# Performance work log

Measured on AMD Instinct MI355X. Metric: run time of the kernel, lower is better.

## Reference

```python
import jax, jax.numpy as jnp
import numpy as np

LN_EPS = 1e-5


def setup_inputs() -> dict:
    key = jax.random.key(0)
    ks = jax.random.split(key, 8)
    B, L, d_model = 2, 2048, 1024
    d_inner, d_state, dt_rank, d_conv = 2048, 16, 64, 4
    f32 = jnp.float32
    A_init = jnp.broadcast_to(jnp.arange(1, d_state + 1, dtype=f32), (d_inner, d_state))
    return {
        "x": jax.random.normal(ks[0], (B, L, d_model), f32),
        "norm_g": jnp.ones((d_model,), f32),
        "norm_b": jnp.zeros((d_model,), f32),
        "in_w": jax.random.normal(ks[1], (2 * d_inner, d_model), f32) / np.sqrt(d_model),
        "conv_w": jax.random.normal(ks[2], (d_inner, 1, d_conv), f32) / np.sqrt(d_conv),
        "conv_b": jnp.zeros((d_inner,), f32),
        "xproj_w": jax.random.normal(ks[3], (dt_rank + 2 * d_state, d_inner), f32) / np.sqrt(d_inner),
        "dt_w": jax.random.normal(ks[4], (d_inner, dt_rank), f32) / np.sqrt(dt_rank),
        "dt_b": jax.random.uniform(ks[5], (d_inner,), f32, np.log(1e-4), np.log(0.1)),
        "A_log": jnp.log(A_init),
        "D": jnp.ones((d_inner,), f32),
        "out_w": jax.random.normal(ks[6], (d_model, d_inner), f32) / np.sqrt(d_inner),
    }


def reference(x, norm_g, norm_b, in_w, conv_w, conv_b, xproj_w, dt_w, dt_b, A_log, D, out_w):
    Bsz, L, d_model = x.shape
    d_inner, d_state = A_log.shape
    dt_rank = dt_w.shape[1]
    d_conv = conv_w.shape[-1]

    residual = x
    # LayerNorm
    mu = jnp.mean(x, axis=-1, keepdims=True)
    var = jnp.var(x, axis=-1, keepdims=True)
    xn = (x - mu) * jax.lax.rsqrt(var + LN_EPS) * norm_g + norm_b

    # in_proj and split into conv/SSM branch x_ and gate z
    xz = xn @ in_w.T                       # (B, L, 2*d_inner)
    x_, z = xz[..., :d_inner], xz[..., d_inner:]

    # causal depthwise conv1d (pad left d_conv-1, truncate to L)
    xp = jnp.pad(x_, ((0, 0), (d_conv - 1, 0), (0, 0)))
    w = conv_w[:, 0, :]                    # (d_inner, d_conv)
    xc = conv_b + sum(xp[:, k:k + L, :] * w[:, k] for k in range(d_conv))
    u = jax.nn.silu(xc)                    # (B, L, d_inner)

    # input-dependent SSM projections
    dbc = u @ xproj_w.T                    # (B, L, dt_rank + 2*d_state)
    delta_raw = dbc[..., :dt_rank]
    Bm = dbc[..., dt_rank:dt_rank + d_state]
    Cm = dbc[..., dt_rank + d_state:]
    delta = jax.nn.softplus(delta_raw @ dt_w.T + dt_b)  # (B, L, d_inner)
    A = -jnp.exp(A_log)                    # (d_inner, d_state), negative

    # selective scan over L (ZOH-discretized recurrence)
    def step(h, ins):
        d_t, B_t, C_t, u_t = ins           # (B,d_inner),(B,N),(B,N),(B,d_inner)
        dA = jnp.exp(d_t[..., None] * A)                 # (B, d_inner, N)
        dB = d_t[..., None] * B_t[:, None, :]            # (B, d_inner, N)
        h = dA * h + dB * u_t[..., None]
        y_t = jnp.einsum('bdn,bn->bd', h, C_t)
        return h, y_t

    h0 = jnp.zeros((Bsz, d_inner, d_state), x.dtype)
    xs = (jnp.swapaxes(delta, 0, 1), jnp.swapaxes(Bm, 0, 1),
          jnp.swapaxes(Cm, 0, 1), jnp.swapaxes(u, 0, 1))
    _, ys = jax.lax.scan(step, h0, xs)     # ys: (L, B, d_inner)
    y = jnp.swapaxes(ys, 0, 1) + u * D

    # gate, out projection, residual (dropout is identity in eval)
    y = y * jax.nn.silu(z)
    return y @ out_w.T + residual
```

## Files before the change

### kernel.cpp

```cpp
#include <hip/hip_runtime.h>
#include <stdint.h>

typedef unsigned short u16;
typedef unsigned int u32;
typedef __attribute__((ext_vector_type(8))) short bf16x8;
typedef __attribute__((ext_vector_type(4))) float f32x4;
typedef __attribute__((ext_vector_type(4))) unsigned short u16x4;

#define DEV static __device__ __forceinline__

DEV u16 f2b(float f) {
  u32 u = __builtin_bit_cast(u32, f);
  u32 r = (u + 0x7fffu + ((u >> 16) & 1u)) >> 16;
  return (u16)r;
}
DEV float b2f(u16 b) {
  u32 u = ((u32)b) << 16;
  return __builtin_bit_cast(float, u);
}

DEV float fexp2(float x) {
#if __has_builtin(__builtin_amdgcn_exp2f)
  return __builtin_amdgcn_exp2f(x);
#else
  float r;
  asm("v_exp_f32 %0, %1" : "=v"(r) : "v"(x));
  return r;
#endif
}
DEV float flog2(float x) {
#if __has_builtin(__builtin_amdgcn_logf)
  return __builtin_amdgcn_logf(x);
#else
  float r;
  asm("v_log_f32 %0, %1" : "=v"(r) : "v"(x));
  return r;
#endif
}
#define L2E 1.44269504f

DEV void gld16(const void* g, void* l) {
  __builtin_amdgcn_global_load_lds(
      (__attribute__((address_space(1))) void*)(void*)(g),
      (__attribute__((address_space(3))) void*)(l), 16, 0, 0);
}

__global__ void cvt_f32_bf16(const float* __restrict__ in, u16* __restrict__ out, int n) {
  int i = blockIdx.x * blockDim.x + threadIdx.x;
  int stride = gridDim.x * blockDim.x;
  for (; i < n; i += stride) out[i] = f2b(in[i]);
}

__global__ void cvt_pad_xproj(const float* __restrict__ in, u16* __restrict__ out) {
  int i = blockIdx.x * blockDim.x + threadIdx.x;
  int n = i >> 11;
  out[i] = (n < 96) ? f2b(in[i]) : (u16)0;
}

__global__ __launch_bounds__(256) void ln_fwd(const float* __restrict__ x,
                                              const float* __restrict__ g,
                                              const float* __restrict__ bb,
                                              u16* __restrict__ xn) {
  int row = blockIdx.x;
  int t = threadIdx.x;
  const float4 v = ((const float4*)(x + (size_t)row * 1024))[t];
  float s = v.x + v.y + v.z + v.w;
  float ss = fmaf(v.x, v.x, fmaf(v.y, v.y, fmaf(v.z, v.z, v.w * v.w)));
  for (int off = 32; off; off >>= 1) {
    s += __shfl_down(s, off);
    ss += __shfl_down(ss, off);
  }
  __shared__ float red[8];
  __shared__ float mv[2];
  int w = t >> 6;
  if ((t & 63) == 0) { red[w] = s; red[4 + w] = ss; }
  __syncthreads();
  if (t == 0) {
    float S = red[0] + red[1] + red[2] + red[3];
    float SS = red[4] + red[5] + red[6] + red[7];
    float mu = S * (1.f / 1024.f);
    float var = SS * (1.f / 1024.f) - mu * mu;
    mv[0] = mu;
    mv[1] = rsqrtf(var + 1e-5f);
  }
  __syncthreads();
  float mu = mv[0], rstd = mv[1];
  float4 gv = ((const float4*)g)[t];
  float4 bv = ((const float4*)bb)[t];
  u16x4 o;
  o.x = f2b((v.x - mu) * rstd * gv.x + bv.x);
  o.y = f2b((v.y - mu) * rstd * gv.y + bv.y);
  o.z = f2b((v.z - mu) * rstd * gv.z + bv.z);
  o.w = f2b((v.w - mu) * rstd * gv.w + bv.w);
  ((u16x4*)(xn + (size_t)row * 1024))[t] = o;
}

template <int EPI>
__global__ __launch_bounds__(256, 2) void gemm_bt(const u16* __restrict__ A,
                                                  const u16* __restrict__ Bw,
                                                  void* __restrict__ Cp,
                                                  const float* __restrict__ aux,
                                                  int M, int N, int K) {
  __shared__ u16 As[128 * 32];
  __shared__ u16 Bs[128 * 32];
  const int t = threadIdx.x;
  const int m0 = blockIdx.y * 128;
  const int n0 = blockIdx.x * 128;
  const int lane = t & 63;
  const int wv = t >> 6;
  const int wr = (wv >> 1) * 64;
  const int wc = (wv & 1) * 64;
  const int fr = lane & 15;
  const int fk = (lane >> 4) * 8;

  const int i0 = t, i1 = t + 256;
  const u16* ga0 = A + (size_t)(m0 + (i0 >> 2)) * K + (i0 & 3) * 8;
  const u16* ga1 = A + (size_t)(m0 + (i1 >> 2)) * K + (i1 & 3) * 8;
  const u16* gb0 = Bw + (size_t)(n0 + (i0 >> 2)) * K + (i0 & 3) * 8;
  const u16* gb1 = Bw + (size_t)(n0 + (i1 >> 2)) * K + (i1 & 3) * 8;
  u16* la0 = &As[i0 * 8];
  u16* la1 = &As[i1 * 8];
  u16* lb0 = &Bs[i0 * 8];
  u16* lb1 = &Bs[i1 * 8];

  f32x4 acc[4][4] = {};

  for (int k0 = 0; k0 < K; k0 += 32) {
    gld16(ga0 + k0, la0);
    gld16(ga1 + k0, la1);
    gld16(gb0 + k0, lb0);
    gld16(gb1 + k0, lb1);
    asm volatile("s_waitcnt vmcnt(0)" ::: "memory");
    __syncthreads();
    bf16x8 av[4], bv[4];
#pragma unroll
    for (int mi = 0; mi < 4; ++mi)
      av[mi] = *(const bf16x8*)&As[(wr + mi * 16 + fr) * 32 + fk];
#pragma unroll
    for (int ni = 0; ni < 4; ++ni)
      bv[ni] = *(const bf16x8*)&Bs[(wc + ni * 16 + fr) * 32 + fk];
#pragma unroll
    for (int mi = 0; mi < 4; ++mi)
#pragma unroll
      for (int ni = 0; ni < 4; ++ni)
        acc[mi][ni] = __builtin_amdgcn_mfma_f32_16x16x32_bf16(av[mi], bv[ni], acc[mi][ni], 0, 0, 0);
    __syncthreads();
  }

  const int orow = (lane >> 4) * 4;
  const int ocol = lane & 15;
#pragma unroll
  for (int mi = 0; mi < 4; ++mi)
#pragma unroll
    for (int ni = 0; ni < 4; ++ni)
#pragma unroll
      for (int r = 0; r < 4; ++r) {
        const int gr = m0 + wr + mi * 16 + orow + r;
        const int gc = n0 + wc + ni * 16 + ocol;
        const size_t off = (size_t)gr * N + gc;
        float v = acc[mi][ni][r];
        if (EPI == 0) {
          ((u16*)Cp)[off] = f2b(v);
        } else if (EPI == 1) {
          ((float*)Cp)[off] = v;
        } else if (EPI == 2) {
          float sx = v + aux[gc];
          float sp = (sx > 30.f) ? sx : 0.69314718f * flog2(1.f + fexp2(sx * L2E));
          ((float*)Cp)[off] = sp;
        } else {
          ((float*)Cp)[off] = v + aux[off];
        }
      }
}

__global__ __launch_bounds__(256, 2) void gemm_xproj_sk(const u16* __restrict__ A,
                                                        const u16* __restrict__ Bw,
                                                        float* __restrict__ part) {
  __shared__ u16 As[128 * 32];
  __shared__ u16 Bs[128 * 32];
  const int K = 2048, N = 128;
  const int t = threadIdx.x;
  const int m0 = blockIdx.y * 128;
  const int z = blockIdx.z;
  const int kbeg = z * 256, kend = kbeg + 256;
  const int lane = t & 63;
  const int wv = t >> 6;
  const int wr = (wv >> 1) * 64;
  const int wc = (wv & 1) * 64;
  const int fr = lane & 15;
  const int fk = (lane >> 4) * 8;

  const int i0 = t, i1 = t + 256;
  const u16* ga0 = A + (size_t)(m0 + (i0 >> 2)) * K + (i0 & 3) * 8;
  const u16* ga1 = A + (size_t)(m0 + (i1 >> 2)) * K + (i1 & 3) * 8;
  const u16* gb0 = Bw + (size_t)(i0 >> 2) * K + (i0 & 3) * 8;
  const u16* gb1 = Bw + (size_t)(i1 >> 2) * K + (i1 & 3) * 8;
  u16* la0 = &As[i0 * 8];
  u16* la1 = &As[i1 * 8];
  u16* lb0 = &Bs[i0 * 8];
  u16* lb1 = &Bs[i1 * 8];

  f32x4 acc[4][4] = {};

  for (int k0 = kbeg; k0 < kend; k0 += 32) {
    gld16(ga0 + k0, la0);
    gld16(ga1 + k0, la1);
    gld16(gb0 + k0, lb0);
    gld16(gb1 + k0, lb1);
    asm volatile("s_waitcnt vmcnt(0)" ::: "memory");
    __syncthreads();
    bf16x8 av[4], bv[4];
#pragma unroll
    for (int mi = 0; mi < 4; ++mi)
      av[mi] = *(const bf16x8*)&As[(wr + mi * 16 + fr) * 32 + fk];
#pragma unroll
    for (int ni = 0; ni < 4; ++ni)
      bv[ni] = *(const bf16x8*)&Bs[(wc + ni * 16 + fr) * 32 + fk];
#pragma unroll
    for (int mi = 0; mi < 4; ++mi)
#pragma unroll
      for (int ni = 0; ni < 4; ++ni)
        acc[mi][ni] = __builtin_amdgcn_mfma_f32_16x16x32_bf16(av[mi], bv[ni], acc[mi][ni], 0, 0, 0);
    __syncthreads();
  }

  const int orow = (lane >> 4) * 4;
  const int ocol = lane & 15;
  float* outp = part + (size_t)z * 4096 * 128;
#pragma unroll
  for (int mi = 0; mi < 4; ++mi)
#pragma unroll
    for (int ni = 0; ni < 4; ++ni)
#pragma unroll
      for (int r = 0; r < 4; ++r) {
        const int gr = m0 + wr + mi * 16 + orow + r;
        const int gc = wc + ni * 16 + ocol;
        outp[(size_t)gr * N + gc] = acc[mi][ni][r];
      }
}

__global__ __launch_bounds__(256) void reduce_xproj(const float* __restrict__ part,
                                                    float* __restrict__ dbc,
                                                    u16* __restrict__ dr) {
  int tid = blockIdx.x * 256 + threadIdx.x;
  int m = tid >> 7, col = tid & 127;
  float s = 0.f;
#pragma unroll
  for (int z = 0; z < 8; ++z) s += part[(size_t)z * 524288 + tid];
  dbc[tid] = s;
  if (col < 64) dr[m * 64 + col] = f2b(s);
}

__global__ __launch_bounds__(256) void conv_silu(const u16* __restrict__ xz,
                                                 const float* __restrict__ cw,
                                                 const float* __restrict__ cb,
                                                 u16* __restrict__ u) {
  int idx = blockIdx.x * 256 + threadIdx.x;
  int m = idx >> 9;
  int d = (idx & 511) << 2;
  int tt = m & 2047;
  float4 w0 = *(const float4*)&cw[(size_t)d * 4];
  float4 w1 = *(const float4*)&cw[(size_t)d * 4 + 4];
  float4 w2 = *(const float4*)&cw[(size_t)d * 4 + 8];
  float4 w3 = *(const float4*)&cw[(size_t)d * 4 + 12];
  float4 cbv = *(const float4*)&cb[d];
  float s0 = cbv.x, s1 = cbv.y, s2 = cbv.z, s3 = cbv.w;
#pragma unroll
  for (int k = 0; k < 4; ++k) {
    int ts = tt + k - 3;
    if (ts < 0) continue;
    u16x4 xv = *(const u16x4*)&xz[((size_t)(m + k - 3)) * 4096 + d];
    float wa = (k == 0) ? w0.x : (k == 1) ? w0.y : (k == 2) ? w0.z : w0.w;
    float wb = (k == 0) ? w1.x : (k == 1) ? w1.y : (k == 2) ? w1.z : w1.w;
    float wc = (k == 0) ? w2.x : (k == 1) ? w2.y : (k == 2) ? w2.z : w2.w;
    float wd = (k == 0) ? w3.x : (k == 1) ? w3.y : (k == 2) ? w3.z : w3.w;
    s0 = fmaf(b2f(xv.x), wa, s0);
    s1 = fmaf(b2f(xv.y), wb, s1);
    s2 = fmaf(b2f(xv.z), wc, s2);
    s3 = fmaf(b2f(xv.w), wd, s3);
  }
  s0 = s0 * __builtin_amdgcn_rcpf(1.f + fexp2(-s0 * L2E));
  s1 = s1 * __builtin_amdgcn_rcpf(1.f + fexp2(-s1 * L2E));
  s2 = s2 * __builtin_amdgcn_rcpf(1.f + fexp2(-s2 * L2E));
  s3 = s3 * __builtin_amdgcn_rcpf(1.f + fexp2(-s3 * L2E));
  u16x4 o;
  o.x = f2b(s0); o.y = f2b(s1); o.z = f2b(s2); o.w = f2b(s3);
  *(u16x4*)&u[(size_t)m * 2048 + d] = o;
}


__global__ __launch_bounds__(256, 4) void scan_pass1(const float* __restrict__ delta,
                                                     const u16* __restrict__ ub,
                                                     const float* __restrict__ dbc,
                                                     const float* __restrict__ A_log,
                                                     float* __restrict__ Sb,
                                                     float* __restrict__ Qb) {
  __shared__ float Bs[32 * 16];
  const int blk = blockIdx.x;
  const int b = blk >> 9;
  const int r = blk & 511;
  const int ch = r >> 3;
  const int g = r & 7;
  const int t = threadIdx.x;
  const int d = g * 256 + t;
  const size_t mbase = (size_t)b * 2048 + (size_t)ch * 32;
  {
    int row = t >> 3, pr = t & 7;
    const float2 v = *(const float2*)&dbc[(mbase + row) * 128 + 64 + pr * 2];
    *(float2*)&Bs[row * 16 + pr * 2] = v;
  }
  float AvL2E[16];
  {
    const float4* ap = (const float4*)(A_log + (size_t)d * 16);
#pragma unroll
    for (int q = 0; q < 4; ++q) {
      float4 a = ap[q];
      AvL2E[q * 4 + 0] = -__expf(a.x) * L2E;
      AvL2E[q * 4 + 1] = -__expf(a.y) * L2E;
      AvL2E[q * 4 + 2] = -__expf(a.z) * L2E;
      AvL2E[q * 4 + 3] = -__expf(a.w) * L2E;
    }
  }
  const float* dptr = delta + mbase * 2048 + d;
  const u16* uptr = ub + mbase * 2048 + d;
  float h[16];
#pragma unroll
  for (int n = 0; n < 16; ++n) h[n] = 0.f;
  float S = 0.f;
  __syncthreads();
#pragma unroll 4
  for (int i = 0; i < 32; ++i) {
    float dt = dptr[(size_t)i * 2048];
    float uu = b2f(uptr[(size_t)i * 2048]);
    S += dt;
    float c = dt * uu;
    f32x4 B0 = *(const f32x4*)&Bs[i * 16 + 0];
    f32x4 B1 = *(const f32x4*)&Bs[i * 16 + 4];
    f32x4 B2 = *(const f32x4*)&Bs[i * 16 + 8];
    f32x4 B3 = *(const f32x4*)&Bs[i * 16 + 12];
#pragma unroll
    for (int n = 0; n < 4; ++n) {
      h[n] = fmaf(fexp2(dt * AvL2E[n]), h[n], c * B0[n]);
      h[4 + n] = fmaf(fexp2(dt * AvL2E[4 + n]), h[4 + n], c * B1[n]);
      h[8 + n] = fmaf(fexp2(dt * AvL2E[8 + n]), h[8 + n], c * B2[n]);
      h[12 + n] = fmaf(fexp2(dt * AvL2E[12 + n]), h[12 + n], c * B3[n]);
    }
  }
  const size_t o = (((size_t)ch * 2 + b) * 2048 + d) * 16;
  float4* qp = (float4*)(Qb + o);
  qp[0] = make_float4(h[0], h[1], h[2], h[3]);
  qp[1] = make_float4(h[4], h[5], h[6], h[7]);
  qp[2] = make_float4(h[8], h[9], h[10], h[11]);
  qp[3] = make_float4(h[12], h[13], h[14], h[15]);
  Sb[((size_t)ch * 2 + b) * 2048 + d] = S;
}

__global__ __launch_bounds__(256) void scan_pass2(const float* __restrict__ A_log,
                                                  const float* __restrict__ Sb,
                                                  float* __restrict__ Qb) {
  const int tid = blockIdx.x * 256 + threadIdx.x;
  const int n = tid & 15;
  const int dd = (tid >> 4) & 2047;
  const int b = tid >> 15;
  const float AvL2E = -__expf(A_log[dd * 16 + n]) * L2E;
  float carry = 0.f;
  float Sc = Sb[(size_t)b * 2048 + dd];
  float Qc = Qb[((size_t)b * 2048 + dd) * 16 + n];
  for (int j = 0; j < 64; ++j) {
    float Sn = 0.f, Qn = 0.f;
    if (j + 1 < 64) {
      Sn = Sb[((size_t)(j + 1) * 2 + b) * 2048 + dd];
      Qn = Qb[(((size_t)(j + 1) * 2 + b) * 2048 + dd) * 16 + n];
    }
    float P = fexp2(AvL2E * Sc);
    Qb[(((size_t)j * 2 + b) * 2048 + dd) * 16 + n] = carry;
    carry = fmaf(P, carry, Qc);
    Sc = Sn;
    Qc = Qn;
  }
}

__global__ __launch_bounds__(256, 4) void scan_pass3(const float* __restrict__ delta,
                                                     const u16* __restrict__ ub,
                                                     const float* __restrict__ dbc,
                                                     const u16* __restrict__ xz,
                                                     const float* __restrict__ A_log,
                                                     const float* __restrict__ Dp,
                                                     const float* __restrict__ Qb,
                                                     u16* __restrict__ yg) {
  __shared__ float BCs[32 * 32];
  const int blk = blockIdx.x;
  const int b = blk >> 9;
  const int r = blk & 511;
  const int ch = r >> 3;
  const int g = r & 7;
  const int t = threadIdx.x;
  const int d = g * 256 + t;
  const size_t mbase = (size_t)b * 2048 + (size_t)ch * 32;
  {
    int row = t >> 3, q = t & 7;
    const float4 v = *(const float4*)&dbc[(mbase + row) * 128 + 64 + q * 4];
    *(float4*)&BCs[row * 32 + q * 4] = v;
  }
  float AvL2E[16];
  {
    const float4* ap = (const float4*)(A_log + (size_t)d * 16);
#pragma unroll
    for (int q = 0; q < 4; ++q) {
      float4 a = ap[q];
      AvL2E[q * 4 + 0] = -__expf(a.x) * L2E;
      AvL2E[q * 4 + 1] = -__expf(a.y) * L2E;
      AvL2E[q * 4 + 2] = -__expf(a.z) * L2E;
      AvL2E[q * 4 + 3] = -__expf(a.w) * L2E;
    }
  }
  const float Dvv = Dp[d];
  const float* dptr = delta + mbase * 2048 + d;
  const u16* uptr = ub + mbase * 2048 + d;
  const u16* zptr = xz + mbase * 4096 + 2048 + d;
  u16* yptr = yg + mbase * 2048 + d;
  float h[16];
  {
    const f32x4* qp = (const f32x4*)(Qb + (((size_t)ch * 2 + b) * 2048 + d) * 16);
    f32x4 q0 = qp[0], q1 = qp[1], q2 = qp[2], q3 = qp[3];
#pragma unroll
    for (int n = 0; n < 4; ++n) {
      h[n] = q0[n];
      h[4 + n] = q1[n];
      h[8 + n] = q2[n];
      h[12 + n] = q3[n];
    }
  }
  __syncthreads();
#pragma unroll 4
  for (int i = 0; i < 32; ++i) {
    float dt = dptr[(size_t)i * 2048];
    float uu = b2f(uptr[(size_t)i * 2048]);
    float zz = b2f(zptr[(size_t)i * 4096]);
    float c = dt * uu;
    f32x4 B0 = *(const f32x4*)&BCs[i * 32 + 0];
    f32x4 B1 = *(const f32x4*)&BCs[i * 32 + 4];
    f32x4 B2 = *(const f32x4*)&BCs[i * 32 + 8];
    f32x4 B3 = *(const f32x4*)&BCs[i * 32 + 12];
    f32x4 C0 = *(const f32x4*)&BCs[i * 32 + 16];
    f32x4 C1 = *(const f32x4*)&BCs[i * 32 + 20];
    f32x4 C2 = *(const f32x4*)&BCs[i * 32 + 24];
    f32x4 C3 = *(const f32x4*)&BCs[i * 32 + 28];
    float p0 = 0.f, p1 = 0.f, p2 = 0.f, p3 = 0.f;
#pragma unroll
    for (int n = 0; n < 4; ++n) {
      h[n] = fmaf(fexp2(dt * AvL2E[n]), h[n], c * B0[n]);
      p0 = fmaf(h[n], C0[n], p0);
      h[4 + n] = fmaf(fexp2(dt * AvL2E[4 + n]), h[4 + n], c * B1[n]);
      p1 = fmaf(h[4 + n], C1[n], p1);
      h[8 + n] = fmaf(fexp2(dt * AvL2E[8 + n]), h[8 + n], c * B2[n]);
      p2 = fmaf(h[8 + n], C2[n], p2);
      h[12 + n] = fmaf(fexp2(dt * AvL2E[12 + n]), h[12 + n], c * B3[n]);
      p3 = fmaf(h[12 + n], C3[n], p3);
    }
    float p = (p0 + p1) + (p2 + p3);
    float sz = zz * __builtin_amdgcn_rcpf(1.f + fexp2(-zz * L2E));
    float y = (p + uu * Dvv) * sz;
    yptr[(size_t)i * 2048] = f2b(y);
  }
}

extern "C" void kernel_launch(void* const* d_in, const int* in_sizes, int n_in,
                              void* d_out, int out_size, void* d_ws, size_t ws_size,
                              hipStream_t stream) {
  (void)in_sizes; (void)n_in; (void)out_size; (void)ws_size;
  const float* x = (const float*)d_in[0];
  const float* norm_g = (const float*)d_in[1];
  const float* norm_b = (const float*)d_in[2];
  const float* in_w = (const float*)d_in[3];
  const float* conv_w = (const float*)d_in[4];
  const float* conv_b = (const float*)d_in[5];
  const float* xproj_w = (const float*)d_in[6];
  const float* dt_w = (const float*)d_in[7];
  const float* dt_b = (const float*)d_in[8];
  const float* A_log = (const float*)d_in[9];
  const float* Dv = (const float*)d_in[10];
  const float* out_w = (const float*)d_in[11];
  float* out = (float*)d_out;

  char* p = (char*)d_ws;
  auto alloc = [&](size_t bytes) {
    char* r = p;
    p += (bytes + 255) & ~(size_t)255;
    return r;
  };
  u16* xn = (u16*)alloc(4096ull * 1024 * 2);
  u16* inw_b = (u16*)alloc(4096ull * 1024 * 2);
  u16* xz_b = (u16*)alloc(4096ull * 4096 * 2);
  u16* u_b = (u16*)alloc(4096ull * 2048 * 2);
  u16* xpw_b = (u16*)alloc(128ull * 2048 * 2);
  float* dbc = (float*)alloc(4096ull * 128 * 4);
  u16* dr_b = (u16*)alloc(4096ull * 64 * 2);
  u16* dtw_b = (u16*)alloc(2048ull * 64 * 2);
  float* dl = (float*)alloc(4096ull * 2048 * 4);
  u16* yg_b = (u16*)alloc(4096ull * 2048 * 2);
  u16* outw_b = (u16*)alloc(1024ull * 2048 * 2);
  float* Sb = (float*)alloc(64ull * 2 * 2048 * 4);
  float* Qb = (float*)alloc(64ull * 2 * 2048 * 16 * 4);

  cvt_f32_bf16<<<2048, 256, 0, stream>>>(in_w, inw_b, 4096 * 1024);
  cvt_f32_bf16<<<2048, 256, 0, stream>>>(out_w, outw_b, 1024 * 2048);
  cvt_f32_bf16<<<512, 256, 0, stream>>>(dt_w, dtw_b, 2048 * 64);
  cvt_pad_xproj<<<1024, 256, 0, stream>>>(xproj_w, xpw_b);

  ln_fwd<<<4096, 256, 0, stream>>>(x, norm_g, norm_b, xn);
  gemm_bt<0><<<dim3(32, 32), 256, 0, stream>>>(xn, inw_b, xz_b, nullptr, 4096, 4096, 1024);
  conv_silu<<<8192, 256, 0, stream>>>(xz_b, conv_w, conv_b, u_b);
  gemm_xproj_sk<<<dim3(1, 32, 8), 256, 0, stream>>>(u_b, xpw_b, dl);
  reduce_xproj<<<2048, 256, 0, stream>>>(dl, dbc, dr_b);
  gemm_bt<2><<<dim3(16, 32), 256, 0, stream>>>(dr_b, dtw_b, dl, dt_b, 4096, 2048, 64);
  scan_pass1<<<1024, 256, 0, stream>>>(dl, u_b, dbc, A_log, Sb, Qb);
  scan_pass2<<<256, 256, 0, stream>>>(A_log, Sb, Qb);
  scan_pass3<<<1024, 256, 0, stream>>>(dl, u_b, dbc, xz_b, A_log, Dv, Qb, yg_b);
  gemm_bt<3><<<dim3(8, 32), 256, 0, stream>>>(yg_b, outw_b, out, x, 4096, 1024, 2048);
}
```

Measured before the change: 328.4 us.

## Store delta in bf16, merge weight conversions, narrow out-proj tile

The softplus delta GEMM epilogue now writes bf16 instead of fp32, which halves delta traffic in the write and in both scan passes. The four weight-conversion launches are merged into a single grid-stride kernel. The output-projection GEMM uses a 128x64 tile so it launches 512 blocks instead of 256, improving CU occupancy on the N=1024 projection. The bf16 delta adds rounding error that feeds into the exp/recurrence.

After: 322.2 us. No clear change (-1.9%).

```diff
diff --git a/kernel.cpp b/kernel.cpp
--- a/kernel.cpp
+++ b/kernel.cpp
@@ -45,16 +45,28 @@
       (__attribute__((address_space(3))) void*)(l), 16, 0, 0);
 }
 
-__global__ void cvt_f32_bf16(const float* __restrict__ in, u16* __restrict__ out, int n) {
-  int i = blockIdx.x * blockDim.x + threadIdx.x;
-  int stride = gridDim.x * blockDim.x;
-  for (; i < n; i += stride) out[i] = f2b(in[i]);
-}
-
-__global__ void cvt_pad_xproj(const float* __restrict__ in, u16* __restrict__ out) {
-  int i = blockIdx.x * blockDim.x + threadIdx.x;
-  int n = i >> 11;
-  out[i] = (n < 96) ? f2b(in[i]) : (u16)0;
+__global__ void cvt_all(const float* __restrict__ in_w, const float* __restrict__ out_w,
+                        const float* __restrict__ dt_w, const float* __restrict__ xproj_w,
+                        u16* __restrict__ inw_b, u16* __restrict__ outw_b,
+                        u16* __restrict__ dtw_b, u16* __restrict__ xpw_b) {
+  const int N0 = 4194304, N1 = 2097152, N2 = 131072, N3 = 262144;
+  int i = blockIdx.x * 256 + threadIdx.x;
+  int stride = gridDim.x * 256;
+  for (; i < N0 + N1 + N2 + N3; i += stride) {
+    if (i < N0) {
+      inw_b[i] = f2b(in_w[i]);
+    } else if (i < N0 + N1) {
+      int j = i - N0;
+      outw_b[j] = f2b(out_w[j]);
+    } else if (i < N0 + N1 + N2) {
+      int j = i - N0 - N1;
+      dtw_b[j] = f2b(dt_w[j]);
+    } else {
+      int j = i - N0 - N1 - N2;
+      int n = j >> 11;
+      xpw_b[j] = (n < 96) ? f2b(xproj_w[j]) : (u16)0;
+    }
+  }
 }
 
 __global__ __launch_bounds__(256) void ln_fwd(const float* __restrict__ x,
@@ -95,21 +107,22 @@
   ((u16x4*)(xn + (size_t)row * 1024))[t] = o;
 }
 
-template <int EPI>
+template <int EPI, int NB>
 __global__ __launch_bounds__(256, 2) void gemm_bt(const u16* __restrict__ A,
                                                   const u16* __restrict__ Bw,
                                                   void* __restrict__ Cp,
                                                   const float* __restrict__ aux,
                                                   int M, int N, int K) {
   __shared__ u16 As[128 * 32];
-  __shared__ u16 Bs[128 * 32];
+  __shared__ u16 Bs[NB * 32];
+  constexpr int ACN = NB / 32;
   const int t = threadIdx.x;
   const int m0 = blockIdx.y * 128;
-  const int n0 = blockIdx.x * 128;
+  const int n0 = blockIdx.x * NB;
   const int lane = t & 63;
   const int wv = t >> 6;
   const int wr = (wv >> 1) * 64;
-  const int wc = (wv & 1) * 64;
+  const int wc = (wv & 1) * (NB / 2);
   const int fr = lane & 15;
   const int fk = (lane >> 4) * 8;
 
@@ -117,32 +130,36 @@
   const u16* ga0 = A + (size_t)(m0 + (i0 >> 2)) * K + (i0 & 3) * 8;
   const u16* ga1 = A + (size_t)(m0 + (i1 >> 2)) * K + (i1 & 3) * 8;
   const u16* gb0 = Bw + (size_t)(n0 + (i0 >> 2)) * K + (i0 & 3) * 8;
-  const u16* gb1 = Bw + (size_t)(n0 + (i1 >> 2)) * K + (i1 & 3) * 8;
   u16* la0 = &As[i0 * 8];
   u16* la1 = &As[i1 * 8];
   u16* lb0 = &Bs[i0 * 8];
-  u16* lb1 = &Bs[i1 * 8];
-
-  f32x4 acc[4][4] = {};
+  const u16* gb1 = nullptr;
+  u16* lb1 = nullptr;
+  if constexpr (NB == 128) {
+    gb1 = Bw + (size_t)(n0 + (i1 >> 2)) * K + (i1 & 3) * 8;
+    lb1 = &Bs[i1 * 8];
+  }
+
+  f32x4 acc[4][ACN] = {};
 
   for (int k0 = 0; k0 < K; k0 += 32) {
     gld16(ga0 + k0, la0);
     gld16(ga1 + k0, la1);
     gld16(gb0 + k0, lb0);
-    gld16(gb1 + k0, lb1);
+    if constexpr (NB == 128) gld16(gb1 + k0, lb1);
     asm volatile("s_waitcnt vmcnt(0)" ::: "memory");
     __syncthreads();
-    bf16x8 av[4], bv[4];
+    bf16x8 av[4], bv[ACN];
 #pragma unroll
     for (int mi = 0; mi < 4; ++mi)
       av[mi] = *(const bf16x8*)&As[(wr + mi * 16 + fr) * 32 + fk];
 #pragma unroll
-    for (int ni = 0; ni < 4; ++ni)
+    for (int ni = 0; ni < ACN; ++ni)
       bv[ni] = *(const bf16x8*)&Bs[(wc + ni * 16 + fr) * 32 + fk];
 #pragma unroll
     for (int mi = 0; mi < 4; ++mi)
 #pragma unroll
-      for (int ni = 0; ni < 4; ++ni)
+      for (int ni = 0; ni < ACN; ++ni)
         acc[mi][ni] = __builtin_amdgcn_mfma_f32_16x16x32_bf16(av[mi], bv[ni], acc[mi][ni], 0, 0, 0);
     __syncthreads();
   }
@@ -152,7 +169,7 @@
 #pragma unroll
   for (int mi = 0; mi < 4; ++mi)
 #pragma unroll
-    for (int ni = 0; ni < 4; ++ni)
+    for (int ni = 0; ni < ACN; ++ni)
 #pragma unroll
       for (int r = 0; r < 4; ++r) {
         const int gr = m0 + wr + mi * 16 + orow + r;
@@ -161,14 +178,12 @@
         float v = acc[mi][ni][r];
         if (EPI == 0) {
           ((u16*)Cp)[off] = f2b(v);
-        } else if (EPI == 1) {
-          ((float*)Cp)[off] = v;
-        } else if (EPI == 2) {
+        } else if (EPI == 3) {
+          ((float*)Cp)[off] = v + aux[off];
+        } else if (EPI == 4) {
           float sx = v + aux[gc];
           float sp = (sx > 30.f) ? sx : 0.69314718f * flog2(1.f + fexp2(sx * L2E));
-          ((float*)Cp)[off] = sp;
-        } else {
-          ((float*)Cp)[off] = v + aux[off];
+          ((u16*)Cp)[off] = f2b(sp);
         }
       }
 }
@@ -288,8 +303,7 @@
   *(u16x4*)&u[(size_t)m * 2048 + d] = o;
 }
 
-
-__global__ __launch_bounds__(256, 4) void scan_pass1(const float* __restrict__ delta,
+__global__ __launch_bounds__(256, 4) void scan_pass1(const u16* __restrict__ delta,
                                                      const u16* __restrict__ ub,
                                                      const float* __restrict__ dbc,
                                                      const float* __restrict__ A_log,
@@ -321,7 +335,7 @@
       AvL2E[q * 4 + 3] = -__expf(a.w) * L2E;
     }
   }
-  const float* dptr = delta + mbase * 2048 + d;
+  const u16* dptr = delta + mbase * 2048 + d;
   const u16* uptr = ub + mbase * 2048 + d;
   float h[16];
 #pragma unroll
@@ -330,7 +344,7 @@
   __syncthreads();
 #pragma unroll 4
   for (int i = 0; i < 32; ++i) {
-    float dt = dptr[(size_t)i * 2048];
+    float dt = b2f(dptr[(size_t)i * 2048]);
     float uu = b2f(uptr[(size_t)i * 2048]);
     S += dt;
     float c = dt * uu;
@@ -380,7 +394,7 @@
   }
 }
 
-__global__ __launch_bounds__(256, 4) void scan_pass3(const float* __restrict__ delta,
+__global__ __launch_bounds__(256, 4) void scan_pass3(const u16* __restrict__ delta,
                                                      const u16* __restrict__ ub,
                                                      const float* __restrict__ dbc,
                                                      const u16* __restrict__ xz,
@@ -415,7 +429,7 @@
     }
   }
   const float Dvv = Dp[d];
-  const float* dptr = delta + mbase * 2048 + d;
+  const u16* dptr = delta + mbase * 2048 + d;
   const u16* uptr = ub + mbase * 2048 + d;
   const u16* zptr = xz + mbase * 4096 + 2048 + d;
   u16* yptr = yg + mbase * 2048 + d;
@@ -434,7 +448,7 @@
   __syncthreads();
 #pragma unroll 4
   for (int i = 0; i < 32; ++i) {
-    float dt = dptr[(size_t)i * 2048];
+    float dt = b2f(dptr[(size_t)i * 2048]);
     float uu = b2f(uptr[(size_t)i * 2048]);
     float zz = b2f(zptr[(size_t)i * 4096]);
     float c = dt * uu;
@@ -497,25 +511,23 @@
   float* dbc = (float*)alloc(4096ull * 128 * 4);
   u16* dr_b = (u16*)alloc(4096ull * 64 * 2);
   u16* dtw_b = (u16*)alloc(2048ull * 64 * 2);
-  float* dl = (float*)alloc(4096ull * 2048 * 4);
+  float* dl_f = (float*)alloc(4096ull * 2048 * 4);
+  u16* dl_h = (u16*)dl_f;
   u16* yg_b = (u16*)alloc(4096ull * 2048 * 2);
   u16* outw_b = (u16*)alloc(1024ull * 2048 * 2);
   float* Sb = (float*)alloc(64ull * 2 * 2048 * 4);
   float* Qb = (float*)alloc(64ull * 2 * 2048 * 16 * 4);
 
-  cvt_f32_bf16<<<2048, 256, 0, stream>>>(in_w, inw_b, 4096 * 1024);
-  cvt_f32_bf16<<<2048, 256, 0, stream>>>(out_w, outw_b, 1024 * 2048);
-  cvt_f32_bf16<<<512, 256, 0, stream>>>(dt_w, dtw_b, 2048 * 64);
-  cvt_pad_xproj<<<1024, 256, 0, stream>>>(xproj_w, xpw_b);
+  cvt_all<<<8192, 256, 0, stream>>>(in_w, out_w, dt_w, xproj_w, inw_b, outw_b, dtw_b, xpw_b);
 
   ln_fwd<<<4096, 256, 0, stream>>>(x, norm_g, norm_b, xn);
-  gemm_bt<0><<<dim3(32, 32), 256, 0, stream>>>(xn, inw_b, xz_b, nullptr, 4096, 4096, 1024);
+  gemm_bt<0, 128><<<dim3(32, 32), 256, 0, stream>>>(xn, inw_b, xz_b, nullptr, 4096, 4096, 1024);
   conv_silu<<<8192, 256, 0, stream>>>(xz_b, conv_w, conv_b, u_b);
-  gemm_xproj_sk<<<dim3(1, 32, 8), 256, 0, stream>>>(u_b, xpw_b, dl);
-  reduce_xproj<<<2048, 256, 0, stream>>>(dl, dbc, dr_b);
-  gemm_bt<2><<<dim3(16, 32), 256, 0, stream>>>(dr_b, dtw_b, dl, dt_b, 4096, 2048, 64);
-  scan_pass1<<<1024, 256, 0, stream>>>(dl, u_b, dbc, A_log, Sb, Qb);
+  gemm_xproj_sk<<<dim3(1, 32, 8), 256, 0, stream>>>(u_b, xpw_b, dl_f);
+  reduce_xproj<<<2048, 256, 0, stream>>>(dl_f, dbc, dr_b);
+  gemm_bt<4, 128><<<dim3(16, 32), 256, 0, stream>>>(dr_b, dtw_b, dl_h, dt_b, 4096, 2048, 64);
+  scan_pass1<<<1024, 256, 0, stream>>>(dl_h, u_b, dbc, A_log, Sb, Qb);
   scan_pass2<<<256, 256, 0, stream>>>(A_log, Sb, Qb);
-  scan_pass3<<<1024, 256, 0, stream>>>(dl, u_b, dbc, xz_b, A_log, Dv, Qb, yg_b);
-  gemm_bt<3><<<dim3(8, 32), 256, 0, stream>>>(yg_b, outw_b, out, x, 4096, 1024, 2048);
-}
+  scan_pass3<<<1024, 256, 0, stream>>>(dl_h, u_b, dbc, xz_b, A_log, Dv, Qb, yg_b);
+  gemm_bt<3, 64><<<dim3(16, 32), 256, 0, stream>>>(yg_b, outw_b, out, x, 4096, 1024, 2048);
+}
```
